# Kernel tuning notes

Measured on AMD Instinct MI355X. Metric: run time of the kernel, lower is better.

The kernel has to match this reference:

```python
import jax, jax.numpy as jnp
import numpy as np

B, C, H, W_, N, E = 8, 256, 128, 128, 4096, 128
EPS = 1e-12  # torch F.normalize default eps


def grid_sample_points(x, kpts):
    """Bilinear grid_sample at point coords, padding_mode='zeros', align_corners=False.
    x: [B,C,H,W], kpts: [B,N,2] in [-1,1] (x,y order) -> [B,C,N].
    """
    Bx, Cx, Hx, Wx = x.shape
    # unnormalize (align_corners=False)
    ix = (kpts[..., 0] + 1.0) * (Wx * 0.5) - 0.5  # [B,N]
    iy = (kpts[..., 1] + 1.0) * (Hx * 0.5) - 0.5
    x0f = jnp.floor(ix)
    y0f = jnp.floor(iy)
    wx = ix - x0f  # fractional weights
    wy = iy - y0f
    x0 = x0f.astype(jnp.int32)
    y0 = y0f.astype(jnp.int32)
    x1 = x0 + 1
    y1 = y0 + 1

    def gather(xi, yi):
        valid = (xi >= 0) & (xi < Wx) & (yi >= 0) & (yi < Hx)  # [B,N]
        xc = jnp.clip(xi, 0, Wx - 1)
        yc = jnp.clip(yi, 0, Hx - 1)
        # per-batch gather of [C] vectors at N points -> [B,C,N]
        v = jax.vmap(lambda xb, yy, xx: xb[:, yy, xx])(x, yc, xc)
        return v * valid[:, None, :].astype(x.dtype)

    v00 = gather(x0, y0)
    v10 = gather(x1, y0)
    v01 = gather(x0, y1)
    v11 = gather(x1, y1)
    wxb = wx[:, None, :]
    wyb = wy[:, None, :]
    return (v00 * (1 - wxb) * (1 - wyb)
            + v10 * wxb * (1 - wyb)
            + v01 * (1 - wxb) * wyb
            + v11 * wxb * wyb)


def setup_inputs() -> dict:
    key = jax.random.key(0)
    k1, k2, k3 = jax.random.split(key, 3)
    x = jax.random.normal(k1, (B, C, H, W_), dtype=jnp.float32)
    # keypoints in normalized [-1,1] coords (grid_sample convention)
    kpts = jax.random.uniform(k2, (B, N, 2), dtype=jnp.float32) * 2.0 - 1.0
    # xavier_normal_(gain=0.1) for Linear(C -> E)
    std = 0.1 * np.sqrt(2.0 / (C + E))
    whiten_w = jax.random.normal(k3, (E, C), dtype=jnp.float32) * std
    whiten_b = jnp.zeros((E,), dtype=jnp.float32)
    return {"x": x, "kpts": kpts, "whiten_w": whiten_w, "whiten_b": whiten_b}


def reference(x, kpts, whiten_w, whiten_b):
    desc = grid_sample_points(x, kpts)              # [B,C,N]
    desc = jnp.transpose(desc, (0, 2, 1))           # [B,N,C]
    desc = jnp.einsum('bnc,ec->bne', desc, whiten_w) + whiten_b  # [B,N,E]
    norm = jnp.maximum(jnp.linalg.norm(desc, axis=2, keepdims=True), EPS)
    return desc / norm
```

## Files before the change

### kernel.cpp

```cpp
#include <hip/hip_runtime.h>
#include <hip/hip_bf16.h>
#include <math.h>

#define BB 8
#define CC 256
#define HH 128
#define WW 128
#define NN 4096
#define EE 128

typedef __bf16 bf16x8 __attribute__((ext_vector_type(8)));
typedef float f32x4 __attribute__((ext_vector_type(4)));

#define WF_OFF    0
#define DESCF_OFF 65536
#define WS_NEED   (65536ull + 16777216ull)

__global__ __launch_bounds__(512, 2) void gather_kernel(
    const float* __restrict__ x, const float* __restrict__ kpts,
    const float* __restrict__ W, __bf16* __restrict__ descf,
    __bf16* __restrict__ Wf) {
  __shared__ float buf[2][HH * WW];
  int blk = blockIdx.x;
  int b = blk >> 5, g = blk & 31;
  int t = threadIdx.x;
  const float4* x4 = (const float4*)(x + ((size_t)((b << 8) + (g << 3)) << 14));
  float4 r0[8], r1[8];
#pragma unroll
  for (int q = 0; q < 8; ++q) r0[q] = x4[t + 512 * q];
#pragma unroll
  for (int q = 0; q < 8; ++q) r1[q] = x4[4096 + t + 512 * q];
  if (t < 128) {
    int i = (blk << 7) + t;
    int j = i & 7, lane = (i >> 3) & 63, etile = (i >> 9) & 7, kstep = (i >> 12) & 7;
    Wf[i] = (__bf16)W[(etile * 16 + (lane & 15)) * CC + kstep * 32 + ((lane >> 4) << 3) + j];
  }
  int base[8];
  float4 wt[8];
  const float2* kp = (const float2*)(kpts + ((size_t)(b * NN) << 1));
#pragma unroll
  for (int i = 0; i < 8; ++i) {
    int n = t + (i << 9);
    float2 k2 = kp[n];
    float ix = (k2.x + 1.f) * (WW * 0.5f) - 0.5f;
    float iy = (k2.y + 1.f) * (HH * 0.5f) - 0.5f;
    float x0f = floorf(ix), y0f = floorf(iy);
    float wx = ix - x0f, wy = iy - y0f;
    int x0 = (int)x0f, y0 = (int)y0f;
    float ax0 = (x0 >= 0 && x0 < WW) ? (1.f - wx) : 0.f;
    float ax1 = (x0 + 1 >= 0 && x0 + 1 < WW) ? wx : 0.f;
    float ay0 = (y0 >= 0 && y0 < HH) ? (1.f - wy) : 0.f;
    float ay1 = (y0 + 1 >= 0 && y0 + 1 < HH) ? wy : 0.f;
    int bx = min(max(x0, 0), WW - 2);
    int by = min(max(y0, 0), HH - 2);
    float a0 = 0.f, a1 = 0.f, c0 = 0.f, c1 = 0.f;
    if (x0 == bx) a0 += ax0; else if (x0 == bx + 1) a1 += ax0;
    if (x0 + 1 == bx) a0 += ax1; else if (x0 + 1 == bx + 1) a1 += ax1;
    if (y0 == by) c0 += ay0; else if (y0 == by + 1) c1 += ay0;
    if (y0 + 1 == by) c0 += ay1; else if (y0 + 1 == by + 1) c1 += ay1;
    base[i] = by * WW + bx;
    wt[i] = make_float4(a0 * c0, a1 * c0, a0 * c1, a1 * c1);
  }
  bf16x8 res[8];
#pragma unroll
  for (int p = 0; p < 8; ++p) {
    float* bcur = buf[p & 1];
    float4* b4 = (float4*)bcur;
    if (p & 1) {
#pragma unroll
      for (int q = 0; q < 8; ++q) b4[t + 512 * q] = r1[q];
    } else {
#pragma unroll
      for (int q = 0; q < 8; ++q) b4[t + 512 * q] = r0[q];
    }
    __syncthreads();
    if (p + 2 < 8) {
      if (p & 1) {
#pragma unroll
        for (int q = 0; q < 8; ++q) r1[q] = x4[(p + 2) * 4096 + t + 512 * q];
      } else {
#pragma unroll
        for (int q = 0; q < 8; ++q) r0[q] = x4[(p + 2) * 4096 + t + 512 * q];
      }
    }
#pragma unroll
    for (int i = 0; i < 8; ++i) {
      int bs = base[i];
      float4 w = wt[i];
      float v = bcur[bs] * w.x + bcur[bs + 1] * w.y
              + bcur[bs + WW] * w.z + bcur[bs + WW + 1] * w.w;
      res[i][p] = (__bf16)v;
    }
  }
#pragma unroll
  for (int i = 0; i < 8; ++i) {
    int n = t + (i << 9);
    size_t a16 = ((size_t)b << 17) + ((size_t)(n >> 4) << 9)
               + ((size_t)(g >> 2) << 6) + ((size_t)(g & 3) << 4) + (n & 15);
    *(bf16x8*)(descf + (a16 << 3)) = res[i];
  }
}

__global__ __launch_bounds__(256) void gemm_norm_kernel(
    const __bf16* __restrict__ descf, const __bf16* __restrict__ Wf,
    const float* __restrict__ bias, float* __restrict__ out) {
  __shared__ __bf16 wlds[8 * 8 * 64 * 8];
  int t = threadIdx.x;
  {
    const float4* src = (const float4*)Wf;
    float4* d = (float4*)wlds;
#pragma unroll
    for (int i = 0; i < 16; ++i) d[t + 256 * i] = src[t + 256 * i];
  }
  __syncthreads();
  int blk = blockIdx.x;
  int b = blk >> 6;
  int wave = t >> 6, lane = t & 63;
  int ntile = ((blk & 63) << 2) + wave;
  const bf16x8* bsrc =
      (const bf16x8*)(descf + ((size_t)b << 20) + ((size_t)ntile << 12));
  bf16x8 bfrag[8];
#pragma unroll
  for (int k = 0; k < 8; ++k) bfrag[k] = bsrc[k * 64 + lane];
  const bf16x8* alds = (const bf16x8*)wlds;
  f32x4 acc[8];
#pragma unroll
  for (int e = 0; e < 8; ++e) acc[e] = (f32x4)(0.f);
#pragma unroll
  for (int k = 0; k < 8; ++k) {
#pragma unroll
    for (int e = 0; e < 8; ++e) {
      bf16x8 a = alds[(k * 8 + e) * 64 + lane];
      acc[e] = __builtin_amdgcn_mfma_f32_16x16x32_bf16(a, bfrag[k], acc[e], 0, 0, 0);
    }
  }
  int quad = lane >> 4, col = lane & 15;
  int n = ntile * 16 + col;
  float s = 0.f;
  float4 av[8];
#pragma unroll
  for (int e = 0; e < 8; ++e) {
    float4 bi = *(const float4*)(bias + e * 16 + quad * 4);
    float4 v = make_float4(acc[e][0] + bi.x, acc[e][1] + bi.y,
                           acc[e][2] + bi.z, acc[e][3] + bi.w);
    av[e] = v;
    s += v.x * v.x + v.y * v.y + v.z * v.z + v.w * v.w;
  }
  s += __shfl_xor(s, 16);
  s += __shfl_xor(s, 32);
  float inv = 1.f / fmaxf(sqrtf(s), 1e-12f);
  float4* out4 = (float4*)out + (((size_t)(b * NN + n)) << 5) + quad;
#pragma unroll
  for (int e = 0; e < 8; ++e)
    out4[e * 4] = make_float4(av[e].x * inv, av[e].y * inv,
                              av[e].z * inv, av[e].w * inv);
}

__global__ __launch_bounds__(128) void fused_fallback(
    const float* __restrict__ x, const float* __restrict__ kpts,
    const float* __restrict__ W, const float* __restrict__ bias,
    float* __restrict__ out) {
  __shared__ float dsc[CC];
  __shared__ float sred[2];
  int blk = blockIdx.x;
  int b = blk >> 12;
  float kx = kpts[2 * blk], ky = kpts[2 * blk + 1];
  float ix = (kx + 1.f) * (WW * 0.5f) - 0.5f;
  float iy = (ky + 1.f) * (HH * 0.5f) - 0.5f;
  float x0f = floorf(ix), y0f = floorf(iy);
  float wx = ix - x0f, wy = iy - y0f;
  int x0 = (int)x0f, y0 = (int)y0f;
  float ax0 = (x0 >= 0 && x0 < WW) ? (1.f - wx) : 0.f;
  float ax1 = (x0 + 1 >= 0 && x0 + 1 < WW) ? wx : 0.f;
  float ay0 = (y0 >= 0 && y0 < HH) ? (1.f - wy) : 0.f;
  float ay1 = (y0 + 1 >= 0 && y0 + 1 < HH) ? wy : 0.f;
  int bx = min(max(x0, 0), WW - 2);
  int by = min(max(y0, 0), HH - 2);
  float a0 = 0.f, a1 = 0.f, r0 = 0.f, r1 = 0.f;
  if (x0 == bx) a0 += ax0; else if (x0 == bx + 1) a1 += ax0;
  if (x0 + 1 == bx) a0 += ax1; else if (x0 + 1 == bx + 1) a1 += ax1;
  if (y0 == by) r0 += ay0; else if (y0 == by + 1) r1 += ay0;
  if (y0 + 1 == by) r0 += ay1; else if (y0 + 1 == by + 1) r1 += ay1;
  int base = by * WW + bx;
  float w00 = a0 * r0, w10 = a1 * r0, w01 = a0 * r1, w11 = a1 * r1;
  int t = threadIdx.x;
  const float* src = x + ((size_t)b << 22);
  for (int c = t; c < CC; c += 128) {
    const float* p = src + ((size_t)c << 14);
    dsc[c] = p[base] * w00 + p[base + 1] * w10 + p[base + WW] * w01 + p[base + WW + 1] * w11;
  }
  __syncthreads();
  float acc = bias[t];
  const float* wr = W + t * CC;
  for (int c = 0; c < CC; ++c) acc += wr[c] * dsc[c];
  float s = acc * acc;
  for (int m = 1; m < 64; m <<= 1) s += __shfl_xor(s, m);
  if ((t & 63) == 0) sred[t >> 6] = s;
  __syncthreads();
  float tot = sred[0] + sred[1];
  float inv = 1.f / fmaxf(sqrtf(tot), 1e-12f);
  out[((size_t)blk << 7) + t] = acc * inv;
}

extern "C" void kernel_launch(void* const* d_in, const int* in_sizes, int n_in,
                              void* d_out, int out_size, void* d_ws, size_t ws_size,
                              hipStream_t stream) {
  const float* x    = (const float*)d_in[0];
  const float* kpts = (const float*)d_in[1];
  const float* W    = (const float*)d_in[2];
  const float* bias = (const float*)d_in[3];
  float* out = (float*)d_out;
  if (ws_size >= WS_NEED) {
    char* ws = (char*)d_ws;
    __bf16* Wf    = (__bf16*)(ws + WF_OFF);
    __bf16* descf = (__bf16*)(ws + DESCF_OFF);
    gather_kernel<<<BB * 32, 512, 0, stream>>>(x, kpts, W, descf, Wf);
    gemm_norm_kernel<<<BB * (NN / 64), 256, 0, stream>>>(descf, Wf, bias, out);
  } else {
    fused_fallback<<<BB * NN, 128, 0, stream>>>(x, kpts, W, bias, out);
  }
}
```

Before: 259.7 us.

## Load feature planes via async global-to-LDS copies with single buffer and more blocks

The gather kernel now streams each channel plane directly from global memory into LDS using global_load_lds async copies instead of staging through registers with double buffering. Each block handles 4 channels instead of 8, halving LDS per block (64KB) and doubling the grid to 512 blocks with launch bounds raised to 4 blocks per CU. Outputs are written as 4-wide bf16 fragments into the same MFMA layout. The single buffer needs an extra barrier per plane, so loads no longer overlap the bilinear sampling inside a block; the design relies on more resident blocks to hide latency instead.

```diff
diff --git a/kernel.cpp b/kernel.cpp
--- a/kernel.cpp
+++ b/kernel.cpp
@@ -10,30 +10,39 @@
 #define EE 128
 
 typedef __bf16 bf16x8 __attribute__((ext_vector_type(8)));
+typedef __bf16 bf16x4 __attribute__((ext_vector_type(4)));
 typedef float f32x4 __attribute__((ext_vector_type(4)));
 
 #define WF_OFF    0
 #define DESCF_OFF 65536
 #define WS_NEED   (65536ull + 16777216ull)
 
-__global__ __launch_bounds__(512, 2) void gather_kernel(
+__device__ __forceinline__ void async_copy16(const float* g, float* l) {
+  __builtin_amdgcn_global_load_lds(
+      (const __attribute__((address_space(1))) void*)g,
+      (__attribute__((address_space(3))) void*)l, 16, 0, 0);
+}
+
+__global__ __launch_bounds__(512, 4) void gather_kernel(
     const float* __restrict__ x, const float* __restrict__ kpts,
     const float* __restrict__ W, __bf16* __restrict__ descf,
     __bf16* __restrict__ Wf) {
-  __shared__ float buf[2][HH * WW];
+  __shared__ float plane[HH * WW];
   int blk = blockIdx.x;
-  int b = blk >> 5, g = blk & 31;
+  int b = blk >> 6, g = blk & 63;
   int t = threadIdx.x;
-  const float4* x4 = (const float4*)(x + ((size_t)((b << 8) + (g << 3)) << 14));
-  float4 r0[8], r1[8];
-#pragma unroll
-  for (int q = 0; q < 8; ++q) r0[q] = x4[t + 512 * q];
-#pragma unroll
-  for (int q = 0; q < 8; ++q) r1[q] = x4[4096 + t + 512 * q];
-  if (t < 128) {
+  int w = t >> 6, lane = t & 63;
+  const float* xg = x + ((size_t)((b << 8) + (g << 2)) << 14);
+  {
+    const float* gs = xg + w * 2048 + lane * 4;
+    float* ls = plane + w * 2048;
+#pragma unroll
+    for (int i = 0; i < 8; ++i) async_copy16(gs + i * 256, ls + i * 256);
+  }
+  if (blk < 256 && t < 128) {
     int i = (blk << 7) + t;
-    int j = i & 7, lane = (i >> 3) & 63, etile = (i >> 9) & 7, kstep = (i >> 12) & 7;
-    Wf[i] = (__bf16)W[(etile * 16 + (lane & 15)) * CC + kstep * 32 + ((lane >> 4) << 3) + j];
+    int j = i & 7, ln = (i >> 3) & 63, etile = (i >> 9) & 7, kstep = (i >> 12) & 7;
+    Wf[i] = (__bf16)W[(etile * 16 + (ln & 15)) * CC + kstep * 32 + ((ln >> 4) << 3) + j];
   }
   int base[8];
   float4 wt[8];
@@ -61,43 +70,34 @@
     base[i] = by * WW + bx;
     wt[i] = make_float4(a0 * c0, a1 * c0, a0 * c1, a1 * c1);
   }
-  bf16x8 res[8];
-#pragma unroll
-  for (int p = 0; p < 8; ++p) {
-    float* bcur = buf[p & 1];
-    float4* b4 = (float4*)bcur;
-    if (p & 1) {
-#pragma unroll
-      for (int q = 0; q < 8; ++q) b4[t + 512 * q] = r1[q];
-    } else {
-#pragma unroll
-      for (int q = 0; q < 8; ++q) b4[t + 512 * q] = r0[q];
+  bf16x4 res[8];
+#pragma unroll
+  for (int p = 0; p < 4; ++p) {
+    __syncthreads();
+#pragma unroll
+    for (int i = 0; i < 8; ++i) {
+      int bs = base[i];
+      float4 ww = wt[i];
+      float v = plane[bs] * ww.x + plane[bs + 1] * ww.y
+              + plane[bs + WW] * ww.z + plane[bs + WW + 1] * ww.w;
+      res[i][p] = (__bf16)v;
     }
     __syncthreads();
-    if (p + 2 < 8) {
-      if (p & 1) {
-#pragma unroll
-        for (int q = 0; q < 8; ++q) r1[q] = x4[(p + 2) * 4096 + t + 512 * q];
-      } else {
-#pragma unroll
-        for (int q = 0; q < 8; ++q) r0[q] = x4[(p + 2) * 4096 + t + 512 * q];
-      }
+    if (p < 3) {
+      const float* gs = xg + (p + 1) * 16384 + w * 2048 + lane * 4;
+      float* ls = plane + w * 2048;
+#pragma unroll
+      for (int i = 0; i < 8; ++i) async_copy16(gs + i * 256, ls + i * 256);
     }
-#pragma unroll
-    for (int i = 0; i < 8; ++i) {
-      int bs = base[i];
-      float4 w = wt[i];
-      float v = bcur[bs] * w.x + bcur[bs + 1] * w.y
-              + bcur[bs + WW] * w.z + bcur[bs + WW + 1] * w.w;
-      res[i][p] = (__bf16)v;
-    }
-  }
+  }
+  int c0i = g << 2;
+  int kstep = c0i >> 5, quad = (c0i >> 3) & 3, j0 = c0i & 7;
 #pragma unroll
   for (int i = 0; i < 8; ++i) {
     int n = t + (i << 9);
-    size_t a16 = ((size_t)b << 17) + ((size_t)(n >> 4) << 9)
-               + ((size_t)(g >> 2) << 6) + ((size_t)(g & 3) << 4) + (n & 15);
-    *(bf16x8*)(descf + (a16 << 3)) = res[i];
+    size_t off = (((size_t)((b << 8) + (n >> 4))) << 12)
+               + ((size_t)kstep << 9) + ((size_t)quad << 7) + ((size_t)(n & 15) << 3) + j0;
+    *(bf16x4*)(descf + off) = res[i];
   }
 }
 
@@ -214,7 +214,7 @@
     char* ws = (char*)d_ws;
     __bf16* Wf    = (__bf16*)(ws + WF_OFF);
     __bf16* descf = (__bf16*)(ws + DESCF_OFF);
-    gather_kernel<<<BB * 32, 512, 0, stream>>>(x, kpts, W, descf, Wf);
+    gather_kernel<<<BB * 64, 512, 0, stream>>>(x, kpts, W, descf, Wf);
     gemm_norm_kernel<<<BB * (NN / 64), 256, 0, stream>>>(descf, Wf, bias, out);
   } else {
     fused_fallback<<<BB * NN, 128, 0, stream>>>(x, kpts, W, bias, out);
```

Result: faster. 210.2 us (-19.1%).
